# Kernel tuning notes

Hardware: AMD Instinct MI355X
Metric: run time of the kernel (lower is better)

## Reference

```python
import jax, jax.numpy as jnp
import numpy as np

N_HIDDEN = 8
N_CLASSES = 10
TIME_STEPS = 28
INPUT_DIM = 28
FORGET_BIAS = 1.0


def setup_inputs() -> dict:
    key = jax.random.key(0)
    k1, k2, k3, k4 = jax.random.split(key, 4)
    B = 32768
    x = jax.random.normal(k1, (B, TIME_STEPS, INPUT_DIM), dtype=jnp.float32)
    # BasicLSTMCell kernel: [input_dim + hidden, 4*hidden], gate order i, j, f, o
    W_lstm = jax.random.normal(k2, (INPUT_DIM + N_HIDDEN, 4 * N_HIDDEN), dtype=jnp.float32) * 0.1
    b_lstm = jnp.zeros((4 * N_HIDDEN,), dtype=jnp.float32)  # TF zero-init bias
    out_weights = jax.random.normal(k3, (N_HIDDEN, N_CLASSES), dtype=jnp.float32)
    out_biases = jax.random.normal(k4, (N_CLASSES,), dtype=jnp.float32)
    return {"x": x, "W_lstm": W_lstm, "b_lstm": b_lstm,
            "out_weights": out_weights, "out_biases": out_biases}


def reference(x, W_lstm, b_lstm, out_weights, out_biases):
    B = x.shape[0]

    def step(carry, xt):
        c, h = carry
        gates = jnp.concatenate([xt, h], axis=-1) @ W_lstm + b_lstm  # [B, 4H]
        i, j, f, o = jnp.split(gates, 4, axis=-1)  # BasicLSTMCell order: i, j, f, o
        new_c = c * jax.nn.sigmoid(f + FORGET_BIAS) + jax.nn.sigmoid(i) * jnp.tanh(j)
        new_h = jnp.tanh(new_c) * jax.nn.sigmoid(o)
        return (new_c, new_h), None

    xs = jnp.swapaxes(x, 0, 1)  # [T, B, input_dim]
    init = (jnp.zeros((B, N_HIDDEN), x.dtype), jnp.zeros((B, N_HIDDEN), x.dtype))
    (_, last_h), _ = jax.lax.scan(step, init, xs)
    logits = last_h @ out_weights + out_biases  # [B, n_classes]
    return logits
```

## Files before the change

kernel.cpp:

```cpp
#include <hip/hip_runtime.h>


#define TSTEPS 28
#define DIN    28
#define NH     8
#define NG     32
#define NC     10
#define NROWS  36

__device__ __forceinline__ float fast_exp2(float x) {
    return __builtin_amdgcn_exp2f(x);
}
__device__ __forceinline__ float fast_rcp(float x) {
    return __builtin_amdgcn_rcpf(x);
}
__device__ __forceinline__ float fast_sigmoid(float z) {
    return fast_rcp(1.0f + fast_exp2(-1.4426950408889634f * z));
}
__device__ __forceinline__ float fast_tanh(float z) {
    return 1.0f - 2.0f * fast_rcp(1.0f + fast_exp2(2.8853900817779268f * z));
}

__global__ __launch_bounds__(256, 2) void lstm_kernel(
    const float* __restrict__ x,
    const float* __restrict__ W,
    const float* __restrict__ bias,
    const float* __restrict__ Wout,
    const float* __restrict__ bout,
    float* __restrict__ out)
{
    const int tid   = blockIdx.x * 256 + threadIdx.x;
    const int e     = tid >> 3;
    const int u     = tid & 7;
    const int base8 = (threadIdx.x & 63) & ~7;

    const float* xb = x + (size_t)e * (TSTEPS * DIN);

    float Wr[NROWS][4];
#pragma unroll
    for (int k = 0; k < NROWS; ++k) {
#pragma unroll
        for (int gt = 0; gt < 4; ++gt)
            Wr[k][gt] = W[k * NG + gt * NH + u];
    }
#pragma unroll
    for (int k = 0; k < NROWS; ++k) {
        asm("" : "+v"(Wr[k][0]), "+v"(Wr[k][1]),
                 "+v"(Wr[k][2]), "+v"(Wr[k][3]));
    }

    float bg[4];
#pragma unroll
    for (int gt = 0; gt < 4; ++gt) bg[gt] = bias[gt * NH + u];

    float c = 0.0f;
    float hall[NH];
#pragma unroll
    for (int j = 0; j < NH; ++j) hall[j] = 0.0f;

    float4 xq[2][7];
    {
        const float4* xv = (const float4*)xb;
#pragma unroll
        for (int i = 0; i < 7; ++i) xq[0][i] = xv[i];
    }

    auto do_step = [&](float4 (&cur)[7], float4 (&nxt)[7], int tnext) {
        if (tnext < TSTEPS) {
            const float4* xv = (const float4*)(xb + tnext * DIN);
#pragma unroll
            for (int i = 0; i < 7; ++i) nxt[i] = xv[i];
        }

        float g[4];
#pragma unroll
        for (int gt = 0; gt < 4; ++gt) g[gt] = bg[gt];

#pragma unroll
        for (int i = 0; i < 7; ++i) {
#pragma unroll
            for (int gt = 0; gt < 4; ++gt) {
                g[gt] = fmaf(cur[i].x, Wr[4*i+0][gt], g[gt]);
                g[gt] = fmaf(cur[i].y, Wr[4*i+1][gt], g[gt]);
                g[gt] = fmaf(cur[i].z, Wr[4*i+2][gt], g[gt]);
                g[gt] = fmaf(cur[i].w, Wr[4*i+3][gt], g[gt]);
            }
        }
#pragma unroll
        for (int k = 0; k < NH; ++k) {
#pragma unroll
            for (int gt = 0; gt < 4; ++gt)
                g[gt] = fmaf(hall[k], Wr[DIN + k][gt], g[gt]);
        }

        float ig = fast_sigmoid(g[0]);
        float jg = fast_tanh(g[1]);
        float fg = fast_sigmoid(g[2] + 1.0f);
        float og = fast_sigmoid(g[3]);
        c = c * fg + ig * jg;
        float hu = fast_tanh(c) * og;

#pragma unroll
        for (int j = 0; j < NH; ++j)
            hall[j] = __shfl(hu, base8 + j, 64);
    };

#pragma unroll 1
    for (int tt = 0; tt < TSTEPS; tt += 2) {
        do_step(xq[0], xq[1], tt + 1);
        do_step(xq[1], xq[0], tt + 2);
    }

    float acc = bout[u];
#pragma unroll
    for (int k = 0; k < NH; ++k)
        acc = fmaf(hall[k], Wout[k * NC + u], acc);
    out[(size_t)e * NC + u] = acc;

    if (u < 2) {
        float acc1 = bout[NH + u];
#pragma unroll
        for (int k = 0; k < NH; ++k)
            acc1 = fmaf(hall[k], Wout[k * NC + NH + u], acc1);
        out[(size_t)e * NC + NH + u] = acc1;
    }
}

extern "C" void kernel_launch(void* const* d_in, const int* in_sizes, int n_in,
                              void* d_out, int out_size, void* d_ws, size_t ws_size,
                              hipStream_t stream) {
    const float* x    = (const float*)d_in[0];
    const float* W    = (const float*)d_in[1];
    const float* b    = (const float*)d_in[2];
    const float* Wout = (const float*)d_in[3];
    const float* bout = (const float*)d_in[4];
    float* out = (float*)d_out;

    const int B = in_sizes[0] / (TSTEPS * DIN);
    const int threads = B * NH;
    const int block = 256;
    const int grid = threads / block;
    lstm_kernel<<<grid, block, 0, stream>>>(x, W, b, Wout, bout, out);
}
```

Measured before the change: 179.0 us.

## Assign one thread per gate column and share hidden state via LDS

Each batch element now uses 32 threads, one per gate column, instead of 8 threads that each computed four gates. Gate values are exchanged with xor shuffles, and the new hidden state is broadcast through a small per-group shared-memory buffer instead of eight shuffles. The per-thread weight footprint drops from 144 to 36 registers, which allows a higher launch-bounds occupancy target. In exchange, four times as many threads each load the full x row per step, redundantly, and every thread evaluates all four activations, duplicating that work.

```diff
diff --git a/kernel.cpp b/kernel.cpp
--- a/kernel.cpp
+++ b/kernel.cpp
@@ -21,7 +21,7 @@
     return 1.0f - 2.0f * fast_rcp(1.0f + fast_exp2(2.8853900817779268f * z));
 }
 
-__global__ __launch_bounds__(256, 2) void lstm_kernel(
+__global__ __launch_bounds__(256, 4) void lstm_kernel(
     const float* __restrict__ x,
     const float* __restrict__ W,
     const float* __restrict__ bias,
@@ -29,29 +29,20 @@
     const float* __restrict__ bout,
     float* __restrict__ out)
 {
-    const int tid   = blockIdx.x * 256 + threadIdx.x;
-    const int e     = tid >> 3;
-    const int u     = tid & 7;
-    const int base8 = (threadIdx.x & 63) & ~7;
+    const int tid  = blockIdx.x * 256 + threadIdx.x;
+    const int e    = tid >> 5;
+    const int g    = tid & 31;
+    const int widx = threadIdx.x >> 5;
+
+    __shared__ __align__(16) float hsm[8][NH];
 
     const float* xb = x + (size_t)e * (TSTEPS * DIN);
 
-    float Wr[NROWS][4];
+    float Wc[NROWS];
 #pragma unroll
-    for (int k = 0; k < NROWS; ++k) {
-#pragma unroll
-        for (int gt = 0; gt < 4; ++gt)
-            Wr[k][gt] = W[k * NG + gt * NH + u];
-    }
-#pragma unroll
-    for (int k = 0; k < NROWS; ++k) {
-        asm("" : "+v"(Wr[k][0]), "+v"(Wr[k][1]),
-                 "+v"(Wr[k][2]), "+v"(Wr[k][3]));
-    }
-
-    float bg[4];
-#pragma unroll
-    for (int gt = 0; gt < 4; ++gt) bg[gt] = bias[gt * NH + u];
+    for (int k = 0; k < NROWS; ++k)
+        Wc[k] = W[k * NG + g];
+    const float bg = bias[g];
 
     float c = 0.0f;
     float hall[NH];
@@ -72,37 +63,36 @@
             for (int i = 0; i < 7; ++i) nxt[i] = xv[i];
         }
 
-        float g[4];
-#pragma unroll
-        for (int gt = 0; gt < 4; ++gt) g[gt] = bg[gt];
-
+        float acc = bg;
 #pragma unroll
         for (int i = 0; i < 7; ++i) {
-#pragma unroll
-            for (int gt = 0; gt < 4; ++gt) {
-                g[gt] = fmaf(cur[i].x, Wr[4*i+0][gt], g[gt]);
-                g[gt] = fmaf(cur[i].y, Wr[4*i+1][gt], g[gt]);
-                g[gt] = fmaf(cur[i].z, Wr[4*i+2][gt], g[gt]);
-                g[gt] = fmaf(cur[i].w, Wr[4*i+3][gt], g[gt]);
-            }
+            acc = fmaf(cur[i].x, Wc[4*i+0], acc);
+            acc = fmaf(cur[i].y, Wc[4*i+1], acc);
+            acc = fmaf(cur[i].z, Wc[4*i+2], acc);
+            acc = fmaf(cur[i].w, Wc[4*i+3], acc);
         }
 #pragma unroll
-        for (int k = 0; k < NH; ++k) {
-#pragma unroll
-            for (int gt = 0; gt < 4; ++gt)
-                g[gt] = fmaf(hall[k], Wr[DIN + k][gt], g[gt]);
-        }
+        for (int k = 0; k < NH; ++k)
+            acc = fmaf(hall[k], Wc[DIN + k], acc);
 
-        float ig = fast_sigmoid(g[0]);
-        float jg = fast_tanh(g[1]);
-        float fg = fast_sigmoid(g[2] + 1.0f);
-        float og = fast_sigmoid(g[3]);
+        float v1 = __shfl_xor(acc, 8);
+        float v2 = __shfl_xor(acc, 16);
+        float v3 = __shfl_xor(v1, 16);
+
+        float ig = fast_sigmoid(acc);
+        float jg = fast_tanh(v1);
+        float fg = fast_sigmoid(v2 + 1.0f);
+        float og = fast_sigmoid(v3);
         c = c * fg + ig * jg;
         float hu = fast_tanh(c) * og;
 
-#pragma unroll
-        for (int j = 0; j < NH; ++j)
-            hall[j] = __shfl(hu, base8 + j, 64);
+        if (g < NH) hsm[widx][g] = hu;
+        __builtin_amdgcn_wave_barrier();
+        float4 h01 = *(const float4*)&hsm[widx][0];
+        float4 h23 = *(const float4*)&hsm[widx][4];
+        __builtin_amdgcn_wave_barrier();
+        hall[0] = h01.x; hall[1] = h01.y; hall[2] = h01.z; hall[3] = h01.w;
+        hall[4] = h23.x; hall[5] = h23.y; hall[6] = h23.z; hall[7] = h23.w;
     };
 
 #pragma unroll 1
@@ -111,18 +101,12 @@
         do_step(xq[1], xq[0], tt + 2);
     }
 
-    float acc = bout[u];
-#pragma unroll
-    for (int k = 0; k < NH; ++k)
-        acc = fmaf(hall[k], Wout[k * NC + u], acc);
-    out[(size_t)e * NC + u] = acc;
-
-    if (u < 2) {
-        float acc1 = bout[NH + u];
+    if (g < NC) {
+        float acc = bout[g];
 #pragma unroll
         for (int k = 0; k < NH; ++k)
-            acc1 = fmaf(hall[k], Wout[k * NC + NH + u], acc1);
-        out[(size_t)e * NC + NH + u] = acc1;
+            acc = fmaf(hall[k], Wout[k * NC + g], acc);
+        out[(size_t)e * NC + g] = acc;
     }
 }
 
@@ -137,7 +121,7 @@
     float* out = (float*)d_out;
 
     const int B = in_sizes[0] / (TSTEPS * DIN);
-    const int threads = B * NH;
+    const int threads = B * NG;
     const int block = 256;
     const int grid = threads / block;
     lstm_kernel<<<grid, block, 0, stream>>>(x, W, b, Wout, bout, out);
```

Measured after the change: 253.1 us. +41.4%, slower.
